# Kernel optimization log

Measured on AMD Instinct MI355X. Metric: run time of the kernel, lower is better.

## Reference

```python
import jax, jax.numpy as jnp
import numpy as np

V, H, L, B = 50257, 1024, 10, 256

def setup_inputs() -> dict:
    key = jax.random.key(0)
    ks = jax.random.split(key, 16)
    s = 0.02
    return {
        "tokens": jax.random.randint(ks[0], (1, B), 0, V),
        "hidden": jax.random.normal(ks[1], (1, B, H), jnp.float32),
        "encoder_outputs": jax.random.normal(ks[2], (L, H), jnp.float32),
        "emb": jax.random.normal(ks[3], (V, H), jnp.float32) * s,
        "attn_W": jax.random.normal(ks[4], (L, 2 * H), jnp.float32) * s,
        "attn_b": jnp.zeros((L,), jnp.float32),
        "comb_W": jax.random.normal(ks[5], (H, 2 * H), jnp.float32) * s,
        "comb_b": jnp.zeros((H,), jnp.float32),
        "W_ih": jax.random.normal(ks[6], (3 * H, H), jnp.float32) * s,
        "W_hh": jax.random.normal(ks[7], (3 * H, H), jnp.float32) * s,
        "b_ih": jnp.zeros((3 * H,), jnp.float32),
        "b_hh": jnp.zeros((3 * H,), jnp.float32),
        "out_W": jax.random.normal(ks[8], (V, H), jnp.float32) * s,
        "out_b": jnp.zeros((V,), jnp.float32),
    }

def reference(tokens, hidden, encoder_outputs, emb, attn_W, attn_b, comb_W, comb_b,
              W_ih, W_hh, b_ih, b_hh, out_W, out_b):
    # Embedding lookup (dropout = identity, eval mode)
    embedded = emb[tokens[0]]            # [B, H]
    h = hidden[-1]                       # [B, H]
    # Attention over encoder outputs
    attn_logits = jnp.concatenate([embedded, h], axis=1) @ attn_W.T + attn_b
    attn_weights = jax.nn.softmax(attn_logits, axis=1)          # [B, L]
    attn_applied = attn_weights @ encoder_outputs                # [B, H]
    # Combine + relu -> GRU input
    x = jnp.concatenate([embedded, attn_applied], axis=1) @ comb_W.T + comb_b
    x = jax.nn.relu(x)                   # [B, H]
    # Single GRU step (PyTorch gate ordering: r, z, n)
    gi = x @ W_ih.T + b_ih               # [B, 3H]
    gh = h @ W_hh.T + b_hh               # [B, 3H]
    i_r, i_z, i_n = jnp.split(gi, 3, axis=1)
    h_r, h_z, h_n = jnp.split(gh, 3, axis=1)
    r = jax.nn.sigmoid(i_r + h_r)
    z = jax.nn.sigmoid(i_z + h_z)
    n = jnp.tanh(i_n + r * h_n)
    h_new = (1.0 - z) * n + z * h        # [B, H]
    # Output projection + log_softmax
    output = jax.nn.log_softmax(h_new @ out_W.T + out_b, axis=1)  # [B, V]
    return (output, h_new[None], attn_weights)
```

## Files before the change

kernel.cpp:

```cpp
#include <hip/hip_runtime.h>
#include <hip/hip_bf16.h>
#include <math.h>
#include <stdint.h>

#define B_SZ 256
#define H_SZ 1024
#define L_SZ 10
#define V_SZ 50257

typedef __attribute__((ext_vector_type(8))) short short8;
typedef __attribute__((ext_vector_type(4))) float floatx4;

__device__ __forceinline__ unsigned f2bf_bits(float f) {
    unsigned u = __float_as_uint(f);
    return (u + 0x7FFFu + ((u >> 16) & 1u)) >> 16;
}

__device__ __forceinline__ short8 cvt8(float4 a, float4 b) {
    short8 r;
    r[0] = (short)f2bf_bits(a.x); r[1] = (short)f2bf_bits(a.y);
    r[2] = (short)f2bf_bits(a.z); r[3] = (short)f2bf_bits(a.w);
    r[4] = (short)f2bf_bits(b.x); r[5] = (short)f2bf_bits(b.y);
    r[6] = (short)f2bf_bits(b.z); r[7] = (short)f2bf_bits(b.w);
    return r;
}

#define WSTRIDE 40

template<int MSUB, int RELU>
__global__ __launch_bounds__(256) void gemm_mfma(
    const float* __restrict__ A, const float* __restrict__ W,
    const float* __restrict__ bias, float* __restrict__ C,
    int N, int K)
{
    __shared__ __align__(16) short lwb[64 * WSTRIDE];

    const int tid  = threadIdx.x;
    const int wave = tid >> 6;
    const int lane = tid & 63;
    const int quad = lane >> 4;
    const int l16  = lane & 15;

    const int n0 = blockIdx.x * 64;
    const int m_base = blockIdx.y * (MSUB * 64) + wave * (MSUB * 16);

    const int wr = tid >> 2;
    const int wc = (tid & 3) * 8;
    const bool wvalid = (n0 + wr) < N;
    const float* wp = W + (size_t)(n0 + wr) * K + wc;

    float4 w0 = make_float4(0.f, 0.f, 0.f, 0.f), w1 = w0;
    if (wvalid) { w0 = *(const float4*)wp; w1 = *(const float4*)(wp + 4); }

    const float* arow[MSUB];
#pragma unroll
    for (int ms = 0; ms < MSUB; ++ms)
        arow[ms] = A + (size_t)(m_base + ms * 16 + l16) * K + quad * 8;

    floatx4 zero = {0.f, 0.f, 0.f, 0.f};
    floatx4 acc[MSUB][4];
#pragma unroll
    for (int ms = 0; ms < MSUB; ++ms)
#pragma unroll
        for (int ns = 0; ns < 4; ++ns) acc[ms][ns] = zero;

    for (int k0 = 0; k0 < K; k0 += 32) {
        __syncthreads();
        *(short8*)&lwb[wr * WSTRIDE + wc] = cvt8(w0, w1);
        __syncthreads();
        if (k0 + 32 < K && wvalid) {
            w0 = *(const float4*)(wp + k0 + 32);
            w1 = *(const float4*)(wp + k0 + 36);
        }
        short8 bfrag[4];
#pragma unroll
        for (int ns = 0; ns < 4; ++ns)
            bfrag[ns] = *(const short8*)&lwb[(ns * 16 + l16) * WSTRIDE + quad * 8];
#pragma unroll
        for (int ms = 0; ms < MSUB; ++ms) {
            float4 a0 = *(const float4*)(arow[ms] + k0);
            float4 a1 = *(const float4*)(arow[ms] + k0 + 4);
            short8 afrag = cvt8(a0, a1);
#pragma unroll
            for (int ns = 0; ns < 4; ++ns)
                acc[ms][ns] = __builtin_amdgcn_mfma_f32_16x16x32_bf16(
                    afrag, bfrag[ns], acc[ms][ns], 0, 0, 0);
        }
    }

    float bia[4];
#pragma unroll
    for (int ns = 0; ns < 4; ++ns) {
        int n = n0 + ns * 16 + l16;
        bia[ns] = (n < N) ? bias[n] : 0.f;
    }
#pragma unroll
    for (int ms = 0; ms < MSUB; ++ms) {
        int mb = m_base + ms * 16 + quad * 4;
#pragma unroll
        for (int ns = 0; ns < 4; ++ns) {
            int n = n0 + ns * 16 + l16;
            if (n < N) {
#pragma unroll
                for (int i = 0; i < 4; ++i) {
                    float v = acc[ms][ns][i] + bia[ns];
                    if (RELU) v = fmaxf(v, 0.f);
                    C[(size_t)(mb + i) * N + n] = v;
                }
            }
        }
    }
}

__global__ __launch_bounds__(256) void attn_kernel(
    const int* __restrict__ tokens, const float* __restrict__ hidden,
    const float* __restrict__ enc, const float* __restrict__ emb,
    const float* __restrict__ attn_W, const float* __restrict__ attn_b,
    float* __restrict__ cat_out, float* __restrict__ attn_w_out)
{
    const int b = blockIdx.x;
    const int tid = threadIdx.x;
    const int tok = tokens[b];
    const float* erow = emb + (size_t)tok * H_SZ;
    const float* hrow = hidden + (size_t)b * H_SZ;

    __shared__ float red[L_SZ][256];
    __shared__ float wts[L_SZ];

    float acc[L_SZ];
#pragma unroll
    for (int l = 0; l < L_SZ; ++l) acc[l] = 0.f;

    for (int i = tid; i < H_SZ; i += 256) {
        float e = erow[i];
        float hv = hrow[i];
        cat_out[(size_t)b * 2 * H_SZ + i] = e;
#pragma unroll
        for (int l = 0; l < L_SZ; ++l) {
            acc[l] += e * attn_W[l * 2 * H_SZ + i] + hv * attn_W[l * 2 * H_SZ + H_SZ + i];
        }
    }
#pragma unroll
    for (int l = 0; l < L_SZ; ++l) red[l][tid] = acc[l];
    __syncthreads();
    for (int s = 128; s > 0; s >>= 1) {
        if (tid < s) {
#pragma unroll
            for (int l = 0; l < L_SZ; ++l) red[l][tid] += red[l][tid + s];
        }
        __syncthreads();
    }
    if (tid == 0) {
        float m = -INFINITY;
        float lg[L_SZ];
#pragma unroll
        for (int l = 0; l < L_SZ; ++l) {
            lg[l] = red[l][0] + attn_b[l];
            m = fmaxf(m, lg[l]);
        }
        float s = 0.f;
#pragma unroll
        for (int l = 0; l < L_SZ; ++l) {
            float e = expf(lg[l] - m);
            wts[l] = e;
            s += e;
        }
        float inv = 1.f / s;
#pragma unroll
        for (int l = 0; l < L_SZ; ++l) {
            wts[l] *= inv;
            attn_w_out[(size_t)b * L_SZ + l] = wts[l];
        }
    }
    __syncthreads();

    for (int i = tid; i < H_SZ; i += 256) {
        float s = 0.f;
#pragma unroll
        for (int l = 0; l < L_SZ; ++l) s += wts[l] * enc[l * H_SZ + i];
        cat_out[(size_t)b * 2 * H_SZ + H_SZ + i] = s;
    }
}

__global__ __launch_bounds__(256) void gru_combine(
    const float* __restrict__ gi, const float* __restrict__ gh,
    const float* __restrict__ hidden, float* __restrict__ h_new)
{
    int idx = blockIdx.x * blockDim.x + threadIdx.x;
    if (idx >= B_SZ * H_SZ) return;
    int b = idx >> 10;
    int j = idx & (H_SZ - 1);
    const float* gib = gi + (size_t)b * 3 * H_SZ;
    const float* ghb = gh + (size_t)b * 3 * H_SZ;
    float i_r = gib[j], i_z = gib[H_SZ + j], i_n = gib[2 * H_SZ + j];
    float h_r = ghb[j], h_z = ghb[H_SZ + j], h_n = ghb[2 * H_SZ + j];
    float r = 1.f / (1.f + expf(-(i_r + h_r)));
    float z = 1.f / (1.f + expf(-(i_z + h_z)));
    float n = tanhf(i_n + r * h_n);
    float h = hidden[idx];
    h_new[idx] = (1.f - z) * n + z * h;
}

__global__ __launch_bounds__(1024) void logsoftmax_v2(float* __restrict__ out)
{
    const int b = blockIdx.x;
    float* row = out + (size_t)b * V_SZ;
    const int tid = threadIdx.x;
    const int wave = tid >> 6;
    const int lane = tid & 63;

    const int head = (int)(((16u - ((uintptr_t)row & 15u)) & 15u) >> 2);
    const int nv = (V_SZ - head) >> 2;
    const float4* r4 = (const float4*)(row + head);
    const int tail_start = head + (nv << 2);

    float m = -INFINITY, s = 0.f;
    if (tid < head) {
        float v = row[tid];
        m = v; s = 1.f;
    }
    for (int i = tid; i < nv; i += 1024) {
        float4 v = r4[i];
        float mv = fmaxf(fmaxf(v.x, v.y), fmaxf(v.z, v.w));
        if (mv > m) { s *= expf(m - mv); m = mv; }
        s += expf(v.x - m) + expf(v.y - m) + expf(v.z - m) + expf(v.w - m);
    }
    for (int i = tail_start + tid; i < V_SZ; i += 1024) {
        float v = row[i];
        if (v > m) { s *= expf(m - v); m = v; }
        s += expf(v - m);
    }

    for (int off = 32; off > 0; off >>= 1) {
        float m2 = __shfl_down(m, off);
        float s2 = __shfl_down(s, off);
        float mn = fmaxf(m, m2);
        s = s * expf(m - mn) + s2 * expf(m2 - mn);
        m = mn;
    }
    __shared__ float smax[16], ssum[16], slse;
    if (lane == 0) { smax[wave] = m; ssum[wave] = s; }
    __syncthreads();
    if (tid == 0) {
        float M = smax[0], S = ssum[0];
        for (int w = 1; w < 16; ++w) {
            float mn = fmaxf(M, smax[w]);
            S = S * expf(M - mn) + ssum[w] * expf(smax[w] - mn);
            M = mn;
        }
        slse = M + logf(S);
    }
    __syncthreads();
    const float lse = slse;

    if (tid < head) row[tid] -= lse;
    float4* w4 = (float4*)(row + head);
    for (int i = tid; i < nv; i += 1024) {
        float4 v = r4[i];
        v.x -= lse; v.y -= lse; v.z -= lse; v.w -= lse;
        w4[i] = v;
    }
    for (int i = tail_start + tid; i < V_SZ; i += 1024) row[i] -= lse;
}

extern "C" void kernel_launch(void* const* d_in, const int* in_sizes, int n_in,
                              void* d_out, int out_size, void* d_ws, size_t ws_size,
                              hipStream_t stream)
{
    const int*   tokens = (const int*)d_in[0];
    const float* hidden = (const float*)d_in[1];
    const float* enc    = (const float*)d_in[2];
    const float* emb    = (const float*)d_in[3];
    const float* attn_W = (const float*)d_in[4];
    const float* attn_b = (const float*)d_in[5];
    const float* comb_W = (const float*)d_in[6];
    const float* comb_b = (const float*)d_in[7];
    const float* W_ih   = (const float*)d_in[8];
    const float* W_hh   = (const float*)d_in[9];
    const float* b_ih   = (const float*)d_in[10];
    const float* b_hh   = (const float*)d_in[11];
    const float* out_W  = (const float*)d_in[12];
    const float* out_b  = (const float*)d_in[13];

    float* out = (float*)d_out;
    float* logits     = out;
    float* h_new      = out + (size_t)B_SZ * V_SZ;
    float* attn_w_out = h_new + (size_t)B_SZ * H_SZ;

    float* cat = logits;
    float* x   = cat + (size_t)B_SZ * 2 * H_SZ;
    float* gi  = x   + (size_t)B_SZ * H_SZ;
    float* gh  = gi  + (size_t)B_SZ * 3 * H_SZ;

    attn_kernel<<<B_SZ, 256, 0, stream>>>(tokens, hidden, enc, emb, attn_W, attn_b,
                                          cat, attn_w_out);
    gemm_mfma<1, 1><<<dim3(H_SZ / 64, 4), 256, 0, stream>>>(
        cat, comb_W, comb_b, x, H_SZ, 2 * H_SZ);
    gemm_mfma<1, 0><<<dim3(3 * H_SZ / 64, 4), 256, 0, stream>>>(
        x, W_ih, b_ih, gi, 3 * H_SZ, H_SZ);
    gemm_mfma<1, 0><<<dim3(3 * H_SZ / 64, 4), 256, 0, stream>>>(
        hidden, W_hh, b_hh, gh, 3 * H_SZ, H_SZ);
    gru_combine<<<(B_SZ * H_SZ + 255) / 256, 256, 0, stream>>>(gi, gh, hidden, h_new);
    gemm_mfma<4, 0><<<dim3((V_SZ + 63) / 64, 1), 256, 0, stream>>>(
        h_new, out_W, out_b, logits, V_SZ, H_SZ);
    logsoftmax_v2<<<B_SZ, 1024, 0, stream>>>(logits);
}
```

Before: 700.9 us.

## Double-buffer GEMM weight tiles with deeper prefetch, fuse GRU gemms, prestage bf16 hidden

New measurement: 621.9 us. -11.3%, faster.

```diff
diff --git a/kernel.cpp b/kernel.cpp
--- a/kernel.cpp
+++ b/kernel.cpp
@@ -17,24 +17,25 @@
 }
 
 __device__ __forceinline__ short8 cvt8(float4 a, float4 b) {
-    short8 r;
-    r[0] = (short)f2bf_bits(a.x); r[1] = (short)f2bf_bits(a.y);
-    r[2] = (short)f2bf_bits(a.z); r[3] = (short)f2bf_bits(a.w);
-    r[4] = (short)f2bf_bits(b.x); r[5] = (short)f2bf_bits(b.y);
-    r[6] = (short)f2bf_bits(b.z); r[7] = (short)f2bf_bits(b.w);
-    return r;
+    unsigned r0, r1, r2, r3;
+    asm("v_cvt_pk_bf16_f32 %0, %1, %2" : "=v"(r0) : "v"(a.x), "v"(a.y));
+    asm("v_cvt_pk_bf16_f32 %0, %1, %2" : "=v"(r1) : "v"(a.z), "v"(a.w));
+    asm("v_cvt_pk_bf16_f32 %0, %1, %2" : "=v"(r2) : "v"(b.x), "v"(b.y));
+    asm("v_cvt_pk_bf16_f32 %0, %1, %2" : "=v"(r3) : "v"(b.z), "v"(b.w));
+    union { unsigned u[4]; short8 s; } u;
+    u.u[0] = r0; u.u[1] = r1; u.u[2] = r2; u.u[3] = r3;
+    return u.s;
 }
 
 #define WSTRIDE 40
 
-template<int MSUB, int RELU>
-__global__ __launch_bounds__(256) void gemm_mfma(
-    const float* __restrict__ A, const float* __restrict__ W,
+template<int MSUB, int RELU, int PF, int ABF>
+__device__ __forceinline__ void gemm_body(
+    short (*lwb)[64 * WSTRIDE],
+    const void* __restrict__ A, const float* __restrict__ W,
     const float* __restrict__ bias, float* __restrict__ C,
     int N, int K)
 {
-    __shared__ __align__(16) short lwb[64 * WSTRIDE];
-
     const int tid  = threadIdx.x;
     const int wave = tid >> 6;
     const int lane = tid & 63;
@@ -46,16 +47,20 @@
 
     const int wr = tid >> 2;
     const int wc = (tid & 3) * 8;
-    const bool wvalid = (n0 + wr) < N;
-    const float* wp = W + (size_t)(n0 + wr) * K + wc;
-
-    float4 w0 = make_float4(0.f, 0.f, 0.f, 0.f), w1 = w0;
-    if (wvalid) { w0 = *(const float4*)wp; w1 = *(const float4*)(wp + 4); }
-
-    const float* arow[MSUB];
-#pragma unroll
-    for (int ms = 0; ms < MSUB; ++ms)
-        arow[ms] = A + (size_t)(m_base + ms * 16 + l16) * K + quad * 8;
+    int wrow = n0 + wr;
+    if (wrow >= N) wrow = N - 1;
+    const float* wp = W + (size_t)wrow * K + wc;
+
+    const int nc = K >> 5;
+
+    const float* af[MSUB];
+    const short* ab[MSUB];
+#pragma unroll
+    for (int ms = 0; ms < MSUB; ++ms) {
+        int m = m_base + ms * 16 + l16;
+        if (ABF) ab[ms] = (const short*)A + (size_t)m * K + quad * 8;
+        else     af[ms] = (const float*)A + (size_t)m * K + quad * 8;
+    }
 
     floatx4 zero = {0.f, 0.f, 0.f, 0.f};
     floatx4 acc[MSUB][4];
@@ -64,27 +69,55 @@
 #pragma unroll
         for (int ns = 0; ns < 4; ++ns) acc[ms][ns] = zero;
 
-    for (int k0 = 0; k0 < K; k0 += 32) {
-        __syncthreads();
-        *(short8*)&lwb[wr * WSTRIDE + wc] = cvt8(w0, w1);
-        __syncthreads();
-        if (k0 + 32 < K && wvalid) {
-            w0 = *(const float4*)(wp + k0 + 32);
-            w1 = *(const float4*)(wp + k0 + 36);
-        }
-        short8 bfrag[4];
-#pragma unroll
-        for (int ns = 0; ns < 4; ++ns)
-            bfrag[ns] = *(const short8*)&lwb[(ns * 16 + l16) * WSTRIDE + quad * 8];
-#pragma unroll
-        for (int ms = 0; ms < MSUB; ++ms) {
-            float4 a0 = *(const float4*)(arow[ms] + k0);
-            float4 a1 = *(const float4*)(arow[ms] + k0 + 4);
-            short8 afrag = cvt8(a0, a1);
+    float4 wreg[PF][2];
+#pragma unroll
+    for (int p = 0; p < PF; ++p) {
+        wreg[p][0] = *(const float4*)(wp + p * 32);
+        wreg[p][1] = *(const float4*)(wp + p * 32 + 4);
+    }
+    *(short8*)&lwb[0][wr * WSTRIDE + wc] = cvt8(wreg[0][0], wreg[0][1]);
+    asm volatile("s_waitcnt lgkmcnt(0)" ::: "memory");
+    __builtin_amdgcn_s_barrier();
+
+    for (int c0 = 0; c0 < nc; c0 += PF) {
+#pragma unroll
+        for (int p = 0; p < PF; ++p) {
+            const int c   = c0 + p;
+            const int buf = p & 1;
+
+            if (c + PF < nc) {
+                wreg[p][0] = *(const float4*)(wp + (c + PF) * 32);
+                wreg[p][1] = *(const float4*)(wp + (c + PF) * 32 + 4);
+            }
+
+            short8 bfrag[4];
 #pragma unroll
             for (int ns = 0; ns < 4; ++ns)
-                acc[ms][ns] = __builtin_amdgcn_mfma_f32_16x16x32_bf16(
-                    afrag, bfrag[ns], acc[ms][ns], 0, 0, 0);
+                bfrag[ns] = *(const short8*)&lwb[buf][(ns * 16 + l16) * WSTRIDE + quad * 8];
+#pragma unroll
+            for (int ms = 0; ms < MSUB; ++ms) {
+                short8 afrag;
+                if (ABF) {
+                    afrag = *(const short8*)(ab[ms] + c * 32);
+                } else {
+                    float4 a0 = *(const float4*)(af[ms] + c * 32);
+                    float4 a1 = *(const float4*)(af[ms] + c * 32 + 4);
+                    afrag = cvt8(a0, a1);
+                }
+#pragma unroll
+                for (int ns = 0; ns < 4; ++ns)
+                    acc[ms][ns] = __builtin_amdgcn_mfma_f32_16x16x32_bf16(
+                        afrag, bfrag[ns], acc[ms][ns], 0, 0, 0);
+            }
+
+            if (c + 1 < nc) {
+                const int q = (p + 1 == PF) ? 0 : p + 1;
+                *(short8*)&lwb[buf ^ 1][wr * WSTRIDE + wc] =
+                    cvt8(wreg[q][0], wreg[q][1]);
+            }
+
+            asm volatile("s_waitcnt lgkmcnt(0)" ::: "memory");
+            __builtin_amdgcn_s_barrier();
         }
     }
 
@@ -112,6 +145,32 @@
     }
 }
 
+template<int MSUB, int RELU, int PF, int ABF>
+__global__ __launch_bounds__(256) void gemm_mfma(
+    const void* __restrict__ A, const float* __restrict__ W,
+    const float* __restrict__ bias, float* __restrict__ C,
+    int N, int K)
+{
+    __shared__ __align__(16) short lwb[2][64 * WSTRIDE];
+    gemm_body<MSUB, RELU, PF, ABF>(lwb, A, W, bias, C, N, K);
+}
+
+template<int MSUB, int RELU, int PF>
+__global__ __launch_bounds__(256) void gemm_dual(
+    const void* __restrict__ A0, const float* __restrict__ W0,
+    const float* __restrict__ b0, float* __restrict__ C0,
+    const void* __restrict__ A1, const float* __restrict__ W1,
+    const float* __restrict__ b1, float* __restrict__ C1,
+    int N, int K)
+{
+    __shared__ __align__(16) short lwb[2][64 * WSTRIDE];
+    const void*  A = blockIdx.z ? A1 : A0;
+    const float* W = blockIdx.z ? W1 : W0;
+    const float* b = blockIdx.z ? b1 : b0;
+    float*       C = blockIdx.z ? C1 : C0;
+    gemm_body<MSUB, RELU, PF, 0>(lwb, A, W, b, C, N, K);
+}
+
 __global__ __launch_bounds__(256) void attn_kernel(
     const int* __restrict__ tokens, const float* __restrict__ hidden,
     const float* __restrict__ enc, const float* __restrict__ emb,
@@ -184,7 +243,8 @@
 
 __global__ __launch_bounds__(256) void gru_combine(
     const float* __restrict__ gi, const float* __restrict__ gh,
-    const float* __restrict__ hidden, float* __restrict__ h_new)
+    const float* __restrict__ hidden, float* __restrict__ h_new,
+    short* __restrict__ hb16)
 {
     int idx = blockIdx.x * blockDim.x + threadIdx.x;
     if (idx >= B_SZ * H_SZ) return;
@@ -198,7 +258,9 @@
     float z = 1.f / (1.f + expf(-(i_z + h_z)));
     float n = tanhf(i_n + r * h_n);
     float h = hidden[idx];
-    h_new[idx] = (1.f - z) * n + z * h;
+    float hn = (1.f - z) * n + z * h;
+    h_new[idx] = hn;
+    if (hb16) hb16[idx] = (short)f2bf_bits(hn);
 }
 
 __global__ __launch_bounds__(1024) void logsoftmax_v2(float* __restrict__ out)
@@ -287,21 +349,31 @@
     float* h_new      = out + (size_t)B_SZ * V_SZ;
     float* attn_w_out = h_new + (size_t)B_SZ * H_SZ;
 
-    float* cat = logits;
+    const size_t need = (size_t)B_SZ * H_SZ * 9 * sizeof(float)
+                      + (size_t)B_SZ * H_SZ * sizeof(short);
+    const bool use_ws = (d_ws != nullptr) && (ws_size >= need);
+
+    float* scratch = use_ws ? (float*)d_ws : logits;
+    float* cat = scratch;
     float* x   = cat + (size_t)B_SZ * 2 * H_SZ;
     float* gi  = x   + (size_t)B_SZ * H_SZ;
     float* gh  = gi  + (size_t)B_SZ * 3 * H_SZ;
+    short* hb16 = use_ws ? (short*)(gh + (size_t)B_SZ * 3 * H_SZ) : nullptr;
 
     attn_kernel<<<B_SZ, 256, 0, stream>>>(tokens, hidden, enc, emb, attn_W, attn_b,
                                           cat, attn_w_out);
-    gemm_mfma<1, 1><<<dim3(H_SZ / 64, 4), 256, 0, stream>>>(
+    gemm_mfma<1, 1, 4, 0><<<dim3(H_SZ / 64, 4), 256, 0, stream>>>(
         cat, comb_W, comb_b, x, H_SZ, 2 * H_SZ);
-    gemm_mfma<1, 0><<<dim3(3 * H_SZ / 64, 4), 256, 0, stream>>>(
-        x, W_ih, b_ih, gi, 3 * H_SZ, H_SZ);
-    gemm_mfma<1, 0><<<dim3(3 * H_SZ / 64, 4), 256, 0, stream>>>(
+    gemm_dual<1, 0, 4><<<dim3(3 * H_SZ / 64, 4, 2), 256, 0, stream>>>(
+        x, W_ih, b_ih, gi,
         hidden, W_hh, b_hh, gh, 3 * H_SZ, H_SZ);
-    gru_combine<<<(B_SZ * H_SZ + 255) / 256, 256, 0, stream>>>(gi, gh, hidden, h_new);
-    gemm_mfma<4, 0><<<dim3((V_SZ + 63) / 64, 1), 256, 0, stream>>>(
-        h_new, out_W, out_b, logits, V_SZ, H_SZ);
+    gru_combine<<<(B_SZ * H_SZ + 255) / 256, 256, 0, stream>>>(gi, gh, hidden,
+                                                               h_new, hb16);
+    if (use_ws)
+        gemm_mfma<4, 0, 2, 1><<<dim3((V_SZ + 63) / 64, 1), 256, 0, stream>>>(
+            (const void*)hb16, out_W, out_b, logits, V_SZ, H_SZ);
+    else
+        gemm_mfma<4, 0, 2, 0><<<dim3((V_SZ + 63) / 64, 1), 256, 0, stream>>>(
+            (const void*)h_new, out_W, out_b, logits, V_SZ, H_SZ);
     logsoftmax_v2<<<B_SZ, 1024, 0, stream>>>(logits);
 }
```
